# Kernel tuning notes

Hardware: AMD Instinct MI355X
Metric: run time of the kernel (lower is better)

The kernel has to match this reference:

```python
import jax, jax.numpy as jnp
import numpy as np


def setup_inputs() -> dict:
    key = jax.random.key(0)
    k1, k2, k3 = jax.random.split(key, 3)
    B, C, H, W = 8, 256, 64, 64
    l = jax.random.normal(k1, (B, C, H, W), dtype=jnp.float32)
    # 1x1 conv weights [out=C//2, in=C]; scale 1/sqrt(C) so projected features have ~unit variance
    scale = 1.0 / np.sqrt(C)
    w_theta = jax.random.normal(k2, (C // 2, C), dtype=jnp.float32) * scale
    w_phi = jax.random.normal(k3, (C // 2, C), dtype=jnp.float32) * scale
    return {"l": l, "w_theta": w_theta, "w_phi": w_phi}


def reference(l, w_theta, w_phi):
    # NonLocalOp forward with embed=True, softmax=True
    B, C, H, W = l.shape
    E = w_theta.shape[0]  # C // 2
    HW = H * W
    # 1x1 convs == per-pixel linear maps
    theta = jnp.einsum('bchw,ec->behw', l, w_theta).reshape(B, E, HW)  # [B,E,HW]
    phi = jnp.einsum('bchw,ec->behw', l, w_phi).reshape(B, E, HW)      # [B,E,HW]
    g = l.reshape(B, C, HW)                                            # [B,C,HW]
    # scores: theta^T phi over embed channels, scaled by sqrt(C//2)
    scale = 1.0 / jnp.sqrt(jnp.asarray(C // 2, dtype=l.dtype))
    f = jnp.einsum('beq,bek->bqk', theta, phi) * scale                 # [B,HW,HW]
    f = jax.nn.softmax(f, axis=-1)
    out = jnp.einsum('bqk,bck->bcq', f, g).reshape(B, C, H, W)
    return out
```

## Files before the change

### kernel.cpp

```cpp
#include <hip/hip_runtime.h>
#include <stdint.h>

#define NB 8
#define NC 256
#define NE 128
#define NHW 4096

typedef __bf16 v8bf __attribute__((ext_vector_type(8)));
typedef float v4f __attribute__((ext_vector_type(4)));
typedef float v16f __attribute__((ext_vector_type(16)));
typedef unsigned int v4u __attribute__((ext_vector_type(4)));
typedef unsigned int v2u __attribute__((ext_vector_type(2)));

typedef unsigned int __attribute__((address_space(1))) uint_g;
typedef unsigned int __attribute__((address_space(3))) uint_l;

#if __has_builtin(__builtin_amdgcn_exp2f)
#define EXP2F(x) __builtin_amdgcn_exp2f(x)
#else
#define EXP2F(x) exp2f(x)
#endif

#define BARRIER_LDS() asm volatile("s_waitcnt lgkmcnt(0)\n\ts_barrier" ::: "memory")
#define WAIT_VM0()    asm volatile("s_waitcnt vmcnt(0)" ::: "memory")

__device__ __forceinline__ void dma16(const unsigned short* g, unsigned short* l) {
    __builtin_amdgcn_global_load_lds((const uint_g*)g, (uint_l*)l, 16, 0, 0);
}

__device__ __forceinline__ unsigned short f2bf(float x) {
    union { float f; unsigned int u; } v; v.f = x;
    unsigned int r = v.u + 0x7fffu + ((v.u >> 16) & 1u);
    return (unsigned short)(r >> 16);
}

__device__ __forceinline__ unsigned int pack_bf2_ru(float a, float b) {
    union { float f; unsigned int u; } va, vb; va.f = a; vb.f = b;
    return ((va.u + 0x8000u) >> 16) | ((vb.u + 0x8000u) & 0xffff0000u);
}

__global__ __launch_bounds__(256) void cast_w_kernel(const float* __restrict__ wt,
                                                     const float* __restrict__ wp,
                                                     unsigned short* __restrict__ Wbf) {
    int i = blockIdx.x * 256 + threadIdx.x;
    const float QS = 0.08838834764831845f * 1.4426950408889634f;
    float v = (i < 32768) ? wt[i] * QS : wp[i - 32768];
    Wbf[i] = f2bf(v);
}

__global__ __launch_bounds__(256, 2) void proj_kernel(const float* __restrict__ l,
                                                      const unsigned short* __restrict__ Wbf,
                                                      unsigned short* __restrict__ Qbf,
                                                      unsigned short* __restrict__ Kbf,
                                                      unsigned short* __restrict__ Vbf) {
    __shared__ __align__(16) unsigned short A[64][264];
    __shared__ __align__(16) unsigned short Ost[2][32][136];
    const int tid = threadIdx.x;
    const int b = blockIdx.x & 7;
    const int qt = (blockIdx.x >> 3) << 6;
    const float* lb = l + ((size_t)b * NC * NHW + qt);

    for (int s = 0; s < 16; ++s) {
        int f = tid + s * 256;
        int c = f >> 4, j = f & 15;
        float4 v = *(const float4*)(lb + (size_t)c * NHW + j * 4);
        ushort4 o4;
        o4.x = f2bf(v.x); o4.y = f2bf(v.y); o4.z = f2bf(v.z); o4.w = f2bf(v.w);
        A[j * 4 + 0][c] = o4.x;
        A[j * 4 + 1][c] = o4.y;
        A[j * 4 + 2][c] = o4.z;
        A[j * 4 + 3][c] = o4.w;
        *(ushort4*)(Vbf + (size_t)b * NC * NHW + (size_t)c * NHW + qt + j * 4) = o4;
    }
    __syncthreads();

    const int w = tid >> 6, L = tid & 63;
    const int l15 = L & 15, q4 = L >> 4;
    const v4f vz = {0.f, 0.f, 0.f, 0.f};
    v4f acc[4][4];
    for (int mt = 0; mt < 4; ++mt)
        for (int nt = 0; nt < 4; ++nt) acc[mt][nt] = vz;

    for (int kf = 0; kf < 8; ++kf) {
        int kc = kf * 32 + q4 * 8;
        v8bf a[4], bb[4];
        for (int mt = 0; mt < 4; ++mt)
            a[mt] = *(const v8bf*)&A[mt * 16 + l15][kc];
        for (int nt = 0; nt < 4; ++nt)
            bb[nt] = *(const v8bf*)(Wbf + (w * 64 + nt * 16 + l15) * 256 + kc);
        for (int mt = 0; mt < 4; ++mt)
            for (int nt = 0; nt < 4; ++nt)
                acc[mt][nt] = __builtin_amdgcn_mfma_f32_16x16x32_bf16(a[mt], bb[nt], acc[mt][nt], 0, 0, 0);
    }

    const int side = w >> 1;
    const int ebase = (w & 1) * 64;
#pragma unroll
    for (int ph = 0; ph < 2; ++ph) {
        __syncthreads();
#pragma unroll
        for (int mh = 0; mh < 2; ++mh) {
            int mt = ph * 2 + mh;
#pragma unroll
            for (int nt = 0; nt < 4; ++nt)
#pragma unroll
                for (int r = 0; r < 4; ++r) {
                    int q32 = mh * 16 + q4 * 4 + r;
                    Ost[side][q32][ebase + nt * 16 + l15] = f2bf(acc[mt][nt][r]);
                }
        }
        __syncthreads();
#pragma unroll
        for (int s = 0; s < 4; ++s) {
            int idx = tid + s * 256;
            int sd = idx >> 9, rem = idx & 511;
            int r32 = rem >> 4, c8 = rem & 15;
            unsigned short* dst = sd ? Kbf : Qbf;
            int c8s = sd ? (c8 ^ (r32 & 15)) : c8;
            *(uint4*)(dst + ((size_t)b * NHW + qt + ph * 32 + r32) * NE + c8s * 8) =
                *(const uint4*)&Ost[sd][r32][c8 * 8];
        }
    }
}

__global__ __launch_bounds__(512, 2) void attn_kernel(const unsigned short* __restrict__ Qbf,
                                                      const unsigned short* __restrict__ Kbf,
                                                      const unsigned short* __restrict__ Vbf,
                                                      float* __restrict__ out) {
    __shared__ __align__(16) unsigned char smem[66048];
    unsigned short* KuS = (unsigned short*)smem;
    unsigned short* PuS = (unsigned short*)(smem + 32768);
    float* lsumF = (float*)(smem + 65536);

    const int tid = threadIdx.x;
    const int b = blockIdx.x & 7;
    const int q128 = (blockIdx.x >> 3) << 7;
    const int w = tid >> 6;
    const int L = tid & 63;
    const int l31 = L & 31, hi = L >> 5;
    const int x15 = l31 & 15;

    const unsigned short* Kb = Kbf + (size_t)b * NHW * NE;
    const unsigned short* Vb = Vbf + (size_t)b * NC * NHW;

    if (w < 4) {
        float lacc = 0.f;
        v8bf bq[8];
        const unsigned short* qrow = Qbf + ((size_t)b * NHW + q128 + w * 32 + l31) * NE + hi * 8;
#pragma unroll
        for (int ef = 0; ef < 8; ++ef)
            bq[ef] = *(const v8bf*)(qrow + ef * 16);
#pragma unroll
        for (int jj = 0; jj < 4; ++jj) {
            int j = w * 4 + jj;
            dma16(Kb + (size_t)j * 512 + L * 8, KuS + j * 512);
        }
        WAIT_VM0();
        BARRIER_LDS();
#pragma unroll
        for (int jj = 0; jj < 4; ++jj) {
            int j = w * 4 + jj;
            dma16(Kb + (size_t)64 * NE + (size_t)j * 512 + L * 8, KuS + 8192 + j * 512);
        }
        v16f s_prev[2];
        {
            const unsigned short* kub = KuS;
#pragma unroll
            for (int kt = 0; kt < 2; ++kt) {
                v16f sa, sb;
#pragma unroll
                for (int r = 0; r < 16; ++r) { sa[r] = 0.f; sb[r] = 0.f; }
                const unsigned short* krow = kub + (kt * 32 + l31) * 128;
#pragma unroll
                for (int ef = 0; ef < 4; ++ef) {
                    v8bf ak0 = *(const v8bf*)(krow + (((2 * ef + hi) ^ x15) * 8));
                    v8bf ak1 = *(const v8bf*)(krow + (((2 * (ef + 4) + hi) ^ x15) * 8));
                    sa = __builtin_amdgcn_mfma_f32_32x32x16_bf16(ak0, bq[ef], sa, 0, 0, 0);
                    sb = __builtin_amdgcn_mfma_f32_32x32x16_bf16(ak1, bq[ef + 4], sb, 0, 0, 0);
                }
#pragma unroll
                for (int r = 0; r < 16; ++r) s_prev[kt][r] = sa[r] + sb[r];
            }
        }
        WAIT_VM0();
        BARRIER_LDS();

        const int a1 = l31 * 8 + hi * 4;
        const int a2 = (l31 + 32) * 8 + hi * 4;

        for (int it = 0; it < 65; ++it) {
            if (it < 64) {
                const int buf = it & 1;
                if (it <= 61) {
                    const size_t ktn = (size_t)(it + 2) * 64;
#pragma unroll
                    for (int jj = 0; jj < 4; ++jj) {
                        int j = w * 4 + jj;
                        dma16(Kb + ktn * NE + (size_t)j * 512 + L * 8, KuS + buf * 8192 + j * 512);
                    }
                }
                v16f s_new[2];
                if (it <= 62) {
                    const unsigned short* kub = KuS + ((it + 1) & 1) * 8192;
#pragma unroll
                    for (int kt = 0; kt < 2; ++kt) {
                        v16f sa, sb;
#pragma unroll
                        for (int r = 0; r < 16; ++r) { sa[r] = 0.f; sb[r] = 0.f; }
                        const unsigned short* krow = kub + (kt * 32 + l31) * 128;
#pragma unroll
                        for (int ef = 0; ef < 4; ++ef) {
                            v8bf ak0 = *(const v8bf*)(krow + (((2 * ef + hi) ^ x15) * 8));
                            v8bf ak1 = *(const v8bf*)(krow + (((2 * (ef + 4) + hi) ^ x15) * 8));
                            sa = __builtin_amdgcn_mfma_f32_32x32x16_bf16(ak0, bq[ef], sa, 0, 0, 0);
                            sb = __builtin_amdgcn_mfma_f32_32x32x16_bf16(ak1, bq[ef + 4], sb, 0, 0, 0);
                        }
#pragma unroll
                        for (int r = 0; r < 16; ++r) s_new[kt][r] = sa[r] + sb[r];
                    }
                }
#pragma unroll
                for (int kt = 0; kt < 2; ++kt) {
                    float p[16];
#pragma unroll
                    for (int r = 0; r < 16; ++r) p[r] = EXP2F(s_prev[kt][r]);
                    {
                        float t0 = (p[0] + p[1]) + (p[2] + p[3]);
                        float t1 = (p[4] + p[5]) + (p[6] + p[7]);
                        float t2 = (p[8] + p[9]) + (p[10] + p[11]);
                        float t3 = (p[12] + p[13]) + (p[14] + p[15]);
                        lacc += (t0 + t1) + (t2 + t3);
                    }
                    unsigned int pk[8];
#pragma unroll
                    for (int t = 0; t < 8; ++t) pk[t] = pack_bf2_ru(p[2 * t], p[2 * t + 1]);
                    unsigned short* base0 = PuS + buf * 8192 + (w * 4 + kt * 2) * 512;
                    *(v2u*)(base0 + a1)       = (v2u){pk[0], pk[1]};
                    *(v2u*)(base0 + a2)       = (v2u){pk[2], pk[3]};
                    *(v2u*)(base0 + 512 + a1) = (v2u){pk[4], pk[5]};
                    *(v2u*)(base0 + 512 + a2) = (v2u){pk[6], pk[7]};
                }
                if (it <= 62) {
                    s_prev[0] = s_new[0];
                    s_prev[1] = s_new[1];
                }
                WAIT_VM0();
            }
            BARRIER_LDS();
        }
        float tot = lacc + __shfl_xor(lacc, 32);
        if (hi == 0) lsumF[w * 32 + l31] = tot;
        BARRIER_LDS();
    } else {
        const int ci = w - 4;
        v16f o[2][4];
#pragma unroll
        for (int ct = 0; ct < 2; ++ct)
#pragma unroll
            for (int qt = 0; qt < 4; ++qt)
#pragma unroll
                for (int r = 0; r < 16; ++r) o[ct][qt][r] = 0.f;
        const unsigned short* vb0 = Vb + (size_t)(ci * 64 + l31) * NHW + hi * 8;
        const unsigned short* vb1 = Vb + (size_t)(ci * 64 + 32 + l31) * NHW + hi * 8;
        v8bf av[2][4];
#pragma unroll
        for (int kf = 0; kf < 4; ++kf) {
            av[0][kf] = *(const v8bf*)(vb0 + kf * 16);
            av[1][kf] = *(const v8bf*)(vb1 + kf * 16);
        }
        BARRIER_LDS();
        BARRIER_LDS();

        for (int it = 0; it < 65; ++it) {
            if (it > 0) {
                const int pbuf = (it - 1) & 1;
                const unsigned short* pb = PuS + pbuf * 8192 + (hi * 32 + l31) * 8;
#pragma unroll
                for (int qt = 0; qt < 4; ++qt) {
                    v8bf bp[4];
#pragma unroll
                    for (int kf = 0; kf < 4; ++kf)
                        bp[kf] = *(const v8bf*)(pb + (qt * 4 + kf) * 512);
#pragma unroll
                    for (int kf = 0; kf < 4; ++kf) {
                        o[0][qt] = __builtin_amdgcn_mfma_f32_32x32x16_bf16(av[0][kf], bp[kf], o[0][qt], 0, 0, 0);
                        o[1][qt] = __builtin_amdgcn_mfma_f32_32x32x16_bf16(av[1][kf], bp[kf], o[1][qt], 0, 0, 0);
                    }
                }
                const size_t kc0 = (size_t)(it & 63) * 64;
#pragma unroll
                for (int kf = 0; kf < 4; ++kf) {
                    av[0][kf] = *(const v8bf*)(vb0 + kc0 + kf * 16);
                    av[1][kf] = *(const v8bf*)(vb1 + kc0 + kf * 16);
                }
            }
            BARRIER_LDS();
        }
        BARRIER_LDS();
        float inv[4];
#pragma unroll
        for (int qt = 0; qt < 4; ++qt) inv[qt] = 1.0f / lsumF[qt * 32 + l31];
#pragma unroll
        for (int ct = 0; ct < 2; ++ct)
#pragma unroll
            for (int qt = 0; qt < 4; ++qt) {
                float* ob = out + (size_t)b * NC * NHW + q128 + qt * 32 + l31;
#pragma unroll
                for (int r = 0; r < 16; ++r) {
                    int c = ci * 64 + ct * 32 + (r & 3) + 8 * (r >> 2) + 4 * hi;
                    ob[(size_t)c * NHW] = o[ct][qt][r] * inv[qt];
                }
            }
    }
}

extern "C" void kernel_launch(void* const* d_in, const int* in_sizes, int n_in,
                              void* d_out, int out_size, void* d_ws, size_t ws_size,
                              hipStream_t stream) {
    const float* l  = (const float*)d_in[0];
    const float* wt = (const float*)d_in[1];
    const float* wp = (const float*)d_in[2];
    float* out = (float*)d_out;

    char* ws = (char*)d_ws;
    unsigned short* Wbf = (unsigned short*)ws;
    unsigned short* Qbf = (unsigned short*)(ws + 131072);
    unsigned short* Kbf = (unsigned short*)(ws + 131072 + 8388608);
    unsigned short* Vbf = (unsigned short*)(ws + 131072 + 16777216);

    hipLaunchKernelGGL(cast_w_kernel, dim3(256), dim3(256), 0, stream, wt, wp, Wbf);
    hipLaunchKernelGGL(proj_kernel,   dim3(512), dim3(256), 0, stream, l, Wbf, Qbf, Kbf, Vbf);
    hipLaunchKernelGGL(attn_kernel,   dim3(256), dim3(512), 0, stream, Qbf, Kbf, Vbf, out);
}
```

Before: 199.5 us.

## Double the key tile per iteration to halve barrier count in attention

Each pipeline iteration now handles 128 keys instead of 64, so the producer/consumer loop runs 33 times instead of 65 and pays half as many block barriers. The K and P shared buffers double in size, to about 128KB of LDS per block. The QK score computation for the next tile also moves after the exp/pack of the current tile. In the PV consumer, the second half of the V fragments is loaded inside the loop rather than prefetched. The larger LDS footprint likely drops occupancy from 2 blocks per CU to 1.

Measured after the change: 197.9 us. Within noise of the previous version (-0.8%).

```diff
diff --git a/kernel.cpp b/kernel.cpp
--- a/kernel.cpp
+++ b/kernel.cpp
@@ -127,10 +127,10 @@
                                                       const unsigned short* __restrict__ Kbf,
                                                       const unsigned short* __restrict__ Vbf,
                                                       float* __restrict__ out) {
-    __shared__ __align__(16) unsigned char smem[66048];
+    __shared__ __align__(16) unsigned char smem[131584];
     unsigned short* KuS = (unsigned short*)smem;
-    unsigned short* PuS = (unsigned short*)(smem + 32768);
-    float* lsumF = (float*)(smem + 65536);
+    unsigned short* PuS = (unsigned short*)(smem + 65536);
+    float* lsumF = (float*)(smem + 131072);
 
     const int tid = threadIdx.x;
     const int b = blockIdx.x & 7;
@@ -151,22 +151,22 @@
         for (int ef = 0; ef < 8; ++ef)
             bq[ef] = *(const v8bf*)(qrow + ef * 16);
 #pragma unroll
-        for (int jj = 0; jj < 4; ++jj) {
-            int j = w * 4 + jj;
+        for (int jj = 0; jj < 8; ++jj) {
+            int j = w * 8 + jj;
             dma16(Kb + (size_t)j * 512 + L * 8, KuS + j * 512);
         }
         WAIT_VM0();
         BARRIER_LDS();
 #pragma unroll
-        for (int jj = 0; jj < 4; ++jj) {
-            int j = w * 4 + jj;
-            dma16(Kb + (size_t)64 * NE + (size_t)j * 512 + L * 8, KuS + 8192 + j * 512);
-        }
-        v16f s_prev[2];
+        for (int jj = 0; jj < 8; ++jj) {
+            int j = w * 8 + jj;
+            dma16(Kb + (size_t)16384 + j * 512 + L * 8, KuS + 16384 + j * 512);
+        }
+        v16f s_prev[4];
         {
             const unsigned short* kub = KuS;
 #pragma unroll
-            for (int kt = 0; kt < 2; ++kt) {
+            for (int kt = 0; kt < 4; ++kt) {
                 v16f sa, sb;
 #pragma unroll
                 for (int r = 0; r < 16; ++r) { sa[r] = 0.f; sb[r] = 0.f; }
@@ -188,39 +188,19 @@
         const int a1 = l31 * 8 + hi * 4;
         const int a2 = (l31 + 32) * 8 + hi * 4;
 
-        for (int it = 0; it < 65; ++it) {
-            if (it < 64) {
+        for (int it = 0; it < 33; ++it) {
+            if (it < 32) {
                 const int buf = it & 1;
-                if (it <= 61) {
-                    const size_t ktn = (size_t)(it + 2) * 64;
-#pragma unroll
-                    for (int jj = 0; jj < 4; ++jj) {
-                        int j = w * 4 + jj;
-                        dma16(Kb + ktn * NE + (size_t)j * 512 + L * 8, KuS + buf * 8192 + j * 512);
-                    }
-                }
-                v16f s_new[2];
-                if (it <= 62) {
-                    const unsigned short* kub = KuS + ((it + 1) & 1) * 8192;
-#pragma unroll
-                    for (int kt = 0; kt < 2; ++kt) {
-                        v16f sa, sb;
-#pragma unroll
-                        for (int r = 0; r < 16; ++r) { sa[r] = 0.f; sb[r] = 0.f; }
-                        const unsigned short* krow = kub + (kt * 32 + l31) * 128;
-#pragma unroll
-                        for (int ef = 0; ef < 4; ++ef) {
-                            v8bf ak0 = *(const v8bf*)(krow + (((2 * ef + hi) ^ x15) * 8));
-                            v8bf ak1 = *(const v8bf*)(krow + (((2 * (ef + 4) + hi) ^ x15) * 8));
-                            sa = __builtin_amdgcn_mfma_f32_32x32x16_bf16(ak0, bq[ef], sa, 0, 0, 0);
-                            sb = __builtin_amdgcn_mfma_f32_32x32x16_bf16(ak1, bq[ef + 4], sb, 0, 0, 0);
-                        }
-#pragma unroll
-                        for (int r = 0; r < 16; ++r) s_new[kt][r] = sa[r] + sb[r];
-                    }
-                }
-#pragma unroll
-                for (int kt = 0; kt < 2; ++kt) {
+                if (it <= 29) {
+                    const size_t kro = (size_t)(it + 2) * 16384;
+#pragma unroll
+                    for (int jj = 0; jj < 8; ++jj) {
+                        int j = w * 8 + jj;
+                        dma16(Kb + kro + j * 512 + L * 8, KuS + buf * 16384 + j * 512);
+                    }
+                }
+#pragma unroll
+                for (int kt = 0; kt < 4; ++kt) {
                     float p[16];
 #pragma unroll
                     for (int r = 0; r < 16; ++r) p[r] = EXP2F(s_prev[kt][r]);
@@ -234,15 +214,30 @@
                     unsigned int pk[8];
 #pragma unroll
                     for (int t = 0; t < 8; ++t) pk[t] = pack_bf2_ru(p[2 * t], p[2 * t + 1]);
-                    unsigned short* base0 = PuS + buf * 8192 + (w * 4 + kt * 2) * 512;
+                    unsigned short* base0 = PuS + buf * 16384 + (w * 8 + kt * 2) * 512;
                     *(v2u*)(base0 + a1)       = (v2u){pk[0], pk[1]};
                     *(v2u*)(base0 + a2)       = (v2u){pk[2], pk[3]};
                     *(v2u*)(base0 + 512 + a1) = (v2u){pk[4], pk[5]};
                     *(v2u*)(base0 + 512 + a2) = (v2u){pk[6], pk[7]};
                 }
-                if (it <= 62) {
-                    s_prev[0] = s_new[0];
-                    s_prev[1] = s_new[1];
+                if (it <= 30) {
+                    const unsigned short* kub = KuS + ((it + 1) & 1) * 16384;
+#pragma unroll
+                    for (int kt = 0; kt < 4; ++kt) {
+                        v16f sa, sb;
+#pragma unroll
+                        for (int r = 0; r < 16; ++r) { sa[r] = 0.f; sb[r] = 0.f; }
+                        const unsigned short* krow = kub + (kt * 32 + l31) * 128;
+#pragma unroll
+                        for (int ef = 0; ef < 4; ++ef) {
+                            v8bf ak0 = *(const v8bf*)(krow + (((2 * ef + hi) ^ x15) * 8));
+                            v8bf ak1 = *(const v8bf*)(krow + (((2 * (ef + 4) + hi) ^ x15) * 8));
+                            sa = __builtin_amdgcn_mfma_f32_32x32x16_bf16(ak0, bq[ef], sa, 0, 0, 0);
+                            sb = __builtin_amdgcn_mfma_f32_32x32x16_bf16(ak1, bq[ef + 4], sb, 0, 0, 0);
+                        }
+#pragma unroll
+                        for (int r = 0; r < 16; ++r) s_prev[kt][r] = sa[r] + sb[r];
+                    }
                 }
                 WAIT_VM0();
             }
@@ -271,27 +266,46 @@
         BARRIER_LDS();
         BARRIER_LDS();
 
-        for (int it = 0; it < 65; ++it) {
+        for (int it = 0; it < 33; ++it) {
             if (it > 0) {
+                const size_t kcA = (size_t)(it - 1) * 128;
+                v8bf av2[2][4];
+#pragma unroll
+                for (int kf = 0; kf < 4; ++kf) {
+                    av2[0][kf] = *(const v8bf*)(vb0 + kcA + (kf + 4) * 16);
+                    av2[1][kf] = *(const v8bf*)(vb1 + kcA + (kf + 4) * 16);
+                }
                 const int pbuf = (it - 1) & 1;
-                const unsigned short* pb = PuS + pbuf * 8192 + (hi * 32 + l31) * 8;
+                const unsigned short* pb = PuS + pbuf * 16384 + (hi * 32 + l31) * 8;
 #pragma unroll
                 for (int qt = 0; qt < 4; ++qt) {
                     v8bf bp[4];
 #pragma unroll
                     for (int kf = 0; kf < 4; ++kf)
-                        bp[kf] = *(const v8bf*)(pb + (qt * 4 + kf) * 512);
+                        bp[kf] = *(const v8bf*)(pb + (qt * 8 + kf) * 512);
 #pragma unroll
                     for (int kf = 0; kf < 4; ++kf) {
                         o[0][qt] = __builtin_amdgcn_mfma_f32_32x32x16_bf16(av[0][kf], bp[kf], o[0][qt], 0, 0, 0);
                         o[1][qt] = __builtin_amdgcn_mfma_f32_32x32x16_bf16(av[1][kf], bp[kf], o[1][qt], 0, 0, 0);
                     }
                 }
-                const size_t kc0 = (size_t)(it & 63) * 64;
+#pragma unroll
+                for (int qt = 0; qt < 4; ++qt) {
+                    v8bf bp[4];
+#pragma unroll
+                    for (int kf = 0; kf < 4; ++kf)
+                        bp[kf] = *(const v8bf*)(pb + (qt * 8 + 4 + kf) * 512);
+#pragma unroll
+                    for (int kf = 0; kf < 4; ++kf) {
+                        o[0][qt] = __builtin_amdgcn_mfma_f32_32x32x16_bf16(av2[0][kf], bp[kf], o[0][qt], 0, 0, 0);
+                        o[1][qt] = __builtin_amdgcn_mfma_f32_32x32x16_bf16(av2[1][kf], bp[kf], o[1][qt], 0, 0, 0);
+                    }
+                }
+                const size_t kcB = (size_t)(it & 31) * 128;
 #pragma unroll
                 for (int kf = 0; kf < 4; ++kf) {
-                    av[0][kf] = *(const v8bf*)(vb0 + kc0 + kf * 16);
-                    av[1][kf] = *(const v8bf*)(vb1 + kc0 + kf * 16);
+                    av[0][kf] = *(const v8bf*)(vb0 + kcB + kf * 16);
+                    av[1][kf] = *(const v8bf*)(vb1 + kcB + kf * 16);
                 }
             }
             BARRIER_LDS();
```

## Split PV consumer work across eight waves and reorder score MFMAs

Applied to the files above, without the earlier changes.

The attention block grows from 512 to 768 threads, so eight consumer waves each accumulate 32 output channels instead of four waves accumulating 64. This is meant to add PV MFMA parallelism and cut per-wave accumulator registers. The producer waves now compute the next QK scores after writing the current P tile, with the MFMA chains interleaved across the two key tiles. In exchange, every P fragment is read from LDS by twice as many waves. The launch bound of 3 blocks per CU cuts the register budget per thread, which can cause spills, and LDS use may still cap residency at 2 blocks.

Result: no change. 202.5 us (+1.5%).

```diff
diff --git a/kernel.cpp b/kernel.cpp
--- a/kernel.cpp
+++ b/kernel.cpp
@@ -123,7 +123,7 @@
     }
 }
 
-__global__ __launch_bounds__(512, 2) void attn_kernel(const unsigned short* __restrict__ Qbf,
+__global__ __launch_bounds__(768, 3) void attn_kernel(const unsigned short* __restrict__ Qbf,
                                                       const unsigned short* __restrict__ Kbf,
                                                       const unsigned short* __restrict__ Vbf,
                                                       float* __restrict__ out) {
@@ -160,27 +160,29 @@
 #pragma unroll
         for (int jj = 0; jj < 4; ++jj) {
             int j = w * 4 + jj;
-            dma16(Kb + (size_t)64 * NE + (size_t)j * 512 + L * 8, KuS + 8192 + j * 512);
+            dma16(Kb + (size_t)8192 + j * 512 + L * 8, KuS + 8192 + j * 512);
         }
         v16f s_prev[2];
         {
-            const unsigned short* kub = KuS;
-#pragma unroll
-            for (int kt = 0; kt < 2; ++kt) {
-                v16f sa, sb;
-#pragma unroll
-                for (int r = 0; r < 16; ++r) { sa[r] = 0.f; sb[r] = 0.f; }
-                const unsigned short* krow = kub + (kt * 32 + l31) * 128;
-#pragma unroll
-                for (int ef = 0; ef < 4; ++ef) {
+            v16f tmp[2];
+#pragma unroll
+            for (int kt = 0; kt < 2; ++kt)
+#pragma unroll
+                for (int r = 0; r < 16; ++r) { s_prev[kt][r] = 0.f; tmp[kt][r] = 0.f; }
+#pragma unroll
+            for (int ef = 0; ef < 4; ++ef)
+#pragma unroll
+                for (int kt = 0; kt < 2; ++kt) {
+                    const unsigned short* krow = KuS + (kt * 32 + l31) * 128;
                     v8bf ak0 = *(const v8bf*)(krow + (((2 * ef + hi) ^ x15) * 8));
                     v8bf ak1 = *(const v8bf*)(krow + (((2 * (ef + 4) + hi) ^ x15) * 8));
-                    sa = __builtin_amdgcn_mfma_f32_32x32x16_bf16(ak0, bq[ef], sa, 0, 0, 0);
-                    sb = __builtin_amdgcn_mfma_f32_32x32x16_bf16(ak1, bq[ef + 4], sb, 0, 0, 0);
-                }
-#pragma unroll
-                for (int r = 0; r < 16; ++r) s_prev[kt][r] = sa[r] + sb[r];
-            }
+                    s_prev[kt] = __builtin_amdgcn_mfma_f32_32x32x16_bf16(ak0, bq[ef], s_prev[kt], 0, 0, 0);
+                    tmp[kt]    = __builtin_amdgcn_mfma_f32_32x32x16_bf16(ak1, bq[ef + 4], tmp[kt], 0, 0, 0);
+                }
+#pragma unroll
+            for (int kt = 0; kt < 2; ++kt)
+#pragma unroll
+                for (int r = 0; r < 16; ++r) s_prev[kt][r] += tmp[kt][r];
         }
         WAIT_VM0();
         BARRIER_LDS();
@@ -192,31 +194,11 @@
             if (it < 64) {
                 const int buf = it & 1;
                 if (it <= 61) {
-                    const size_t ktn = (size_t)(it + 2) * 64;
+                    const size_t kro = (size_t)(it + 2) * 8192;
 #pragma unroll
                     for (int jj = 0; jj < 4; ++jj) {
                         int j = w * 4 + jj;
-                        dma16(Kb + ktn * NE + (size_t)j * 512 + L * 8, KuS + buf * 8192 + j * 512);
-                    }
-                }
-                v16f s_new[2];
-                if (it <= 62) {
-                    const unsigned short* kub = KuS + ((it + 1) & 1) * 8192;
-#pragma unroll
-                    for (int kt = 0; kt < 2; ++kt) {
-                        v16f sa, sb;
-#pragma unroll
-                        for (int r = 0; r < 16; ++r) { sa[r] = 0.f; sb[r] = 0.f; }
-                        const unsigned short* krow = kub + (kt * 32 + l31) * 128;
-#pragma unroll
-                        for (int ef = 0; ef < 4; ++ef) {
-                            v8bf ak0 = *(const v8bf*)(krow + (((2 * ef + hi) ^ x15) * 8));
-                            v8bf ak1 = *(const v8bf*)(krow + (((2 * (ef + 4) + hi) ^ x15) * 8));
-                            sa = __builtin_amdgcn_mfma_f32_32x32x16_bf16(ak0, bq[ef], sa, 0, 0, 0);
-                            sb = __builtin_amdgcn_mfma_f32_32x32x16_bf16(ak1, bq[ef + 4], sb, 0, 0, 0);
-                        }
-#pragma unroll
-                        for (int r = 0; r < 16; ++r) s_new[kt][r] = sa[r] + sb[r];
+                        dma16(Kb + kro + j * 512 + L * 8, KuS + buf * 8192 + j * 512);
                     }
                 }
 #pragma unroll
@@ -241,8 +223,26 @@
                     *(v2u*)(base0 + 512 + a2) = (v2u){pk[6], pk[7]};
                 }
                 if (it <= 62) {
-                    s_prev[0] = s_new[0];
-                    s_prev[1] = s_new[1];
+                    const unsigned short* kub = KuS + ((it + 1) & 1) * 8192;
+                    v16f tmp[2];
+#pragma unroll
+                    for (int kt = 0; kt < 2; ++kt)
+#pragma unroll
+                        for (int r = 0; r < 16; ++r) { s_prev[kt][r] = 0.f; tmp[kt][r] = 0.f; }
+#pragma unroll
+                    for (int ef = 0; ef < 4; ++ef)
+#pragma unroll
+                        for (int kt = 0; kt < 2; ++kt) {
+                            const unsigned short* krow = kub + (kt * 32 + l31) * 128;
+                            v8bf ak0 = *(const v8bf*)(krow + (((2 * ef + hi) ^ x15) * 8));
+                            v8bf ak1 = *(const v8bf*)(krow + (((2 * (ef + 4) + hi) ^ x15) * 8));
+                            s_prev[kt] = __builtin_amdgcn_mfma_f32_32x32x16_bf16(ak0, bq[ef], s_prev[kt], 0, 0, 0);
+                            tmp[kt]    = __builtin_amdgcn_mfma_f32_32x32x16_bf16(ak1, bq[ef + 4], tmp[kt], 0, 0, 0);
+                        }
+#pragma unroll
+                    for (int kt = 0; kt < 2; ++kt)
+#pragma unroll
+                        for (int r = 0; r < 16; ++r) s_prev[kt][r] += tmp[kt][r];
                 }
                 WAIT_VM0();
             }
@@ -253,21 +253,16 @@
         BARRIER_LDS();
     } else {
         const int ci = w - 4;
-        v16f o[2][4];
-#pragma unroll
-        for (int ct = 0; ct < 2; ++ct)
-#pragma unroll
-            for (int qt = 0; qt < 4; ++qt)
-#pragma unroll
-                for (int r = 0; r < 16; ++r) o[ct][qt][r] = 0.f;
-        const unsigned short* vb0 = Vb + (size_t)(ci * 64 + l31) * NHW + hi * 8;
-        const unsigned short* vb1 = Vb + (size_t)(ci * 64 + 32 + l31) * NHW + hi * 8;
-        v8bf av[2][4];
-#pragma unroll
-        for (int kf = 0; kf < 4; ++kf) {
-            av[0][kf] = *(const v8bf*)(vb0 + kf * 16);
-            av[1][kf] = *(const v8bf*)(vb1 + kf * 16);
-        }
+        v16f o[4];
+#pragma unroll
+        for (int qt = 0; qt < 4; ++qt)
+#pragma unroll
+            for (int r = 0; r < 16; ++r) o[qt][r] = 0.f;
+        const unsigned short* vb0 = Vb + (size_t)(ci * 32 + l31) * NHW + hi * 8;
+        v8bf av[4];
+#pragma unroll
+        for (int kf = 0; kf < 4; ++kf)
+            av[kf] = *(const v8bf*)(vb0 + kf * 16);
         BARRIER_LDS();
         BARRIER_LDS();
 
@@ -276,23 +271,19 @@
                 const int pbuf = (it - 1) & 1;
                 const unsigned short* pb = PuS + pbuf * 8192 + (hi * 32 + l31) * 8;
 #pragma unroll
-                for (int qt = 0; qt < 4; ++qt) {
+                for (int kf = 0; kf < 4; ++kf) {
                     v8bf bp[4];
 #pragma unroll
-                    for (int kf = 0; kf < 4; ++kf)
-                        bp[kf] = *(const v8bf*)(pb + (qt * 4 + kf) * 512);
-#pragma unroll
-                    for (int kf = 0; kf < 4; ++kf) {
-                        o[0][qt] = __builtin_amdgcn_mfma_f32_32x32x16_bf16(av[0][kf], bp[kf], o[0][qt], 0, 0, 0);
-                        o[1][qt] = __builtin_amdgcn_mfma_f32_32x32x16_bf16(av[1][kf], bp[kf], o[1][qt], 0, 0, 0);
-                    }
+                    for (int qt = 0; qt < 4; ++qt)
+                        bp[qt] = *(const v8bf*)(pb + (qt * 4 + kf) * 512);
+#pragma unroll
+                    for (int qt = 0; qt < 4; ++qt)
+                        o[qt] = __builtin_amdgcn_mfma_f32_32x32x16_bf16(av[kf], bp[qt], o[qt], 0, 0, 0);
                 }
                 const size_t kc0 = (size_t)(it & 63) * 64;
 #pragma unroll
-                for (int kf = 0; kf < 4; ++kf) {
-                    av[0][kf] = *(const v8bf*)(vb0 + kc0 + kf * 16);
-                    av[1][kf] = *(const v8bf*)(vb1 + kc0 + kf * 16);
-                }
+                for (int kf = 0; kf < 4; ++kf)
+                    av[kf] = *(const v8bf*)(vb0 + kc0 + kf * 16);
             }
             BARRIER_LDS();
         }
@@ -301,16 +292,14 @@
 #pragma unroll
         for (int qt = 0; qt < 4; ++qt) inv[qt] = 1.0f / lsumF[qt * 32 + l31];
 #pragma unroll
-        for (int ct = 0; ct < 2; ++ct)
-#pragma unroll
-            for (int qt = 0; qt < 4; ++qt) {
-                float* ob = out + (size_t)b * NC * NHW + q128 + qt * 32 + l31;
-#pragma unroll
-                for (int r = 0; r < 16; ++r) {
-                    int c = ci * 64 + ct * 32 + (r & 3) + 8 * (r >> 2) + 4 * hi;
-                    ob[(size_t)c * NHW] = o[ct][qt][r] * inv[qt];
-                }
+        for (int qt = 0; qt < 4; ++qt) {
+            float* ob = out + (size_t)b * NC * NHW + q128 + qt * 32 + l31;
+#pragma unroll
+            for (int r = 0; r < 16; ++r) {
+                int c = ci * 32 + (r & 3) + 8 * (r >> 2) + 4 * hi;
+                ob[(size_t)c * NHW] = o[qt][r] * inv[qt];
             }
+        }
     }
 }
 
@@ -330,5 +319,5 @@
 
     hipLaunchKernelGGL(cast_w_kernel, dim3(256), dim3(256), 0, stream, wt, wp, Wbf);
     hipLaunchKernelGGL(proj_kernel,   dim3(512), dim3(256), 0, stream, l, Wbf, Qbf, Kbf, Vbf);
-    hipLaunchKernelGGL(attn_kernel,   dim3(256), dim3(512), 0, stream, Qbf, Kbf, Vbf, out);
-}
+    hipLaunchKernelGGL(attn_kernel,   dim3(256), dim3(768), 0, stream, Qbf, Kbf, Vbf, out);
+}
```
